# Optimization experiments

Hardware: AMD Instinct MI355X
Metric: run time of the kernel (lower is better)

Reference implementation:

```python
import jax, jax.numpy as jnp
import numpy as np

DECAY = 0.99
EPS = 1e-05


def setup_inputs() -> dict:
    key = jax.random.key(0)
    k1, k2, k3 = jax.random.split(key, 3)
    B, H, W, D, K = 16, 32, 32, 256, 8192
    x = jax.random.normal(k1, (B, H, W, D), dtype=jnp.float32)
    embed = jax.random.normal(k2, (D, K), dtype=jnp.float32)
    cluster_size = jnp.zeros((K,), dtype=jnp.float32)
    embed_avg = jax.random.normal(k3, (D, K), dtype=jnp.float32)
    return {"x": x, "embed": embed, "cluster_size": cluster_size, "embed_avg": embed_avg}


def reference(x, embed, cluster_size, embed_avg):
    D, K = embed.shape
    flat = x.reshape(-1, D)  # (N, D)
    # squared L2 distances: ||f||^2 - 2 f.e + ||e||^2  -> (N, K)
    dist = (flat * flat).sum(1, keepdims=True) - 2.0 * (flat @ embed) + (embed * embed).sum(0, keepdims=True)
    idx = jnp.argmin(dist, axis=1)  # (N,)
    quantize = jnp.take(embed.T, idx, axis=0).reshape(x.shape)  # (B,H,W,D)
    # EMA codebook statistics (training branch)
    onehot_sum = jnp.zeros((K,), dtype=flat.dtype).at[idx].add(1.0)  # (K,)
    embed_sum = jax.ops.segment_sum(flat, idx, num_segments=K).T  # (D, K)
    new_cluster_size = cluster_size * DECAY + (1.0 - DECAY) * onehot_sum
    new_embed_avg = embed_avg * DECAY + (1.0 - DECAY) * embed_sum
    n = new_cluster_size.sum()
    cs = (new_cluster_size + EPS) / (n + K * EPS) * n
    new_embed = new_embed_avg / cs[None, :]
    latent_loss = jnp.mean((jax.lax.stop_gradient(quantize) - x) ** 2)
    quantize_st = x + jax.lax.stop_gradient(quantize - x)  # straight-through
    return quantize_st, latent_loss, new_embed, new_cluster_size, new_embed_avg
```

## Files before the change

kernel.cpp:

```cpp
#include <hip/hip_runtime.h>

constexpr int NROWS = 16384;
constexpr int D     = 256;
constexpr int K     = 8192;

constexpr float DECAY = 0.99f;
constexpr float OMD   = 0.01f;
constexpr float EPSF  = 1e-5f;

constexpr size_t OUT_Q    = 0;
constexpr size_t OUT_LOSS = (size_t)NROWS * D;
constexpr size_t OUT_NE   = OUT_LOSS + 1;
constexpr size_t OUT_NCS  = OUT_NE + (size_t)D * K;
constexpr size_t OUT_NEA  = OUT_NCS + K;

constexpr size_t WS_KEYS  = 0;
constexpr size_t WS_ENORM = WS_KEYS + (size_t)NROWS * 8;
constexpr size_t WS_NSUM  = WS_ENORM + (size_t)K * 4;
constexpr size_t WS_XH    = ((WS_NSUM + 4096) / 4096) * 4096;
constexpr size_t WS_XL    = WS_XH + (size_t)NROWS * D * 2;
constexpr size_t WS_EHT   = WS_XL + (size_t)NROWS * D * 2;
constexpr size_t WS_ELT   = WS_EHT + (size_t)K * D * 2;

typedef unsigned int u32;
typedef unsigned short u16;
typedef unsigned long long u64;
typedef __attribute__((ext_vector_type(8))) short bf16x8;
typedef __attribute__((ext_vector_type(4))) float f32x4;
typedef __attribute__((ext_vector_type(4))) u32 u32x4;
typedef __attribute__((ext_vector_type(2))) u32 u32x2;

__device__ __forceinline__ u16 f2bf(float f) {
    u32 u = __float_as_uint(f);
    u32 r = (u + 0x7FFFu + ((u >> 16) & 1u)) >> 16;
    return (u16)r;
}
__device__ __forceinline__ float bf2f(u16 h) {
    return __uint_as_float((u32)h << 16);
}

__device__ __forceinline__ void gl_lds16(const void* g, void* l) {
    __builtin_amdgcn_global_load_lds(
        (const __attribute__((address_space(1))) u32*)g,
        (__attribute__((address_space(3))) u32*)l, 16, 0, 0);
}

__global__ void split_x_kernel(const float* __restrict__ x,
                               u16* __restrict__ xh, u16* __restrict__ xl) {
    size_t g = (size_t)blockIdx.x * blockDim.x + threadIdx.x;
    float4 v = *(const float4*)&x[g * 4];
    u16 h0 = f2bf(v.x), h1 = f2bf(v.y), h2 = f2bf(v.z), h3 = f2bf(v.w);
    u16 l0 = f2bf(v.x - bf2f(h0)), l1 = f2bf(v.y - bf2f(h1));
    u16 l2 = f2bf(v.z - bf2f(h2)), l3 = f2bf(v.w - bf2f(h3));
    u32x2 hp, lp;
    hp.x = (u32)h0 | ((u32)h1 << 16); hp.y = (u32)h2 | ((u32)h3 << 16);
    lp.x = (u32)l0 | ((u32)l1 << 16); lp.y = (u32)l2 | ((u32)l3 << 16);
    ((u32x2*)xh)[g] = hp;
    ((u32x2*)xl)[g] = lp;
}

__global__ void transpose_split_enorm(const float* __restrict__ embed,
                                      u16* __restrict__ ehT, u16* __restrict__ elT,
                                      float* __restrict__ enorm) {
    __shared__ float tile[64][68];
    const int kBase = blockIdx.x * 64;
    const int t  = threadIdx.x;
    const int dl = t >> 2;
    const int kl = t >> 2;
    const int qq = t & 3;
    float nacc = 0.f;

    for (int dBase = 0; dBase < D; dBase += 64) {
        #pragma unroll
        for (int i = 0; i < 4; ++i) {
            int kk = qq * 16 + i * 4;
            float4 v = *(const float4*)&embed[(size_t)(dBase + dl) * K + kBase + kk];
            tile[dl][kk + 0] = v.x; tile[dl][kk + 1] = v.y;
            tile[dl][kk + 2] = v.z; tile[dl][kk + 3] = v.w;
        }
        __syncthreads();
        u32 hp[8], lp[8];
        float s = 0.f;
        #pragma unroll
        for (int j = 0; j < 16; ++j) {
            float f = tile[qq * 16 + j][kl];
            s = fmaf(f, f, s);
            u16 hb = f2bf(f);
            u16 lb = f2bf(f - bf2f(hb));
            if (j & 1) { hp[j >> 1] |= (u32)hb << 16; lp[j >> 1] |= (u32)lb << 16; }
            else       { hp[j >> 1]  = hb;            lp[j >> 1]  = lb; }
        }
        s += __shfl_down(s, 1);
        s += __shfl_down(s, 2);
        if (qq == 0) nacc += s;

        size_t o = ((size_t)(kBase + kl) * D + dBase + qq * 16) >> 1;
        u32x4 a, b;
        a.x = hp[0]; a.y = hp[1]; a.z = hp[2]; a.w = hp[3];
        b.x = hp[4]; b.y = hp[5]; b.z = hp[6]; b.w = hp[7];
        *(u32x4*)&((u32*)ehT)[o]     = a;
        *(u32x4*)&((u32*)ehT)[o + 4] = b;
        a.x = lp[0]; a.y = lp[1]; a.z = lp[2]; a.w = lp[3];
        b.x = lp[4]; b.y = lp[5]; b.z = lp[6]; b.w = lp[7];
        *(u32x4*)&((u32*)elT)[o]     = a;
        *(u32x4*)&((u32*)elT)[o + 4] = b;
        __syncthreads();
    }
    if (qq == 0) enorm[kBase + kl] = nacc;
}

__global__ void cs_init_sum_kernel(const float* __restrict__ cluster_size,
                                   float* __restrict__ ncs_out,
                                   float* __restrict__ nsum) {
    int i = blockIdx.x * blockDim.x + threadIdx.x;
    float v = cluster_size[i];
    ncs_out[i] = DECAY * v;
    #pragma unroll
    for (int off = 32; off > 0; off >>= 1) v += __shfl_down(v, off);
    __shared__ float wsum[4];
    if ((threadIdx.x & 63) == 0) wsum[threadIdx.x >> 6] = v;
    __syncthreads();
    if (threadIdx.x == 0)
        atomicAdd(nsum, wsum[0] + wsum[1] + wsum[2] + wsum[3]);
}

__global__ __launch_bounds__(512, 2) void dist_argmin_mfma(
        const u16* __restrict__ xh, const u16* __restrict__ xl,
        const u16* __restrict__ ehT, const u16* __restrict__ elT,
        const float* __restrict__ enorm,
        u64* __restrict__ keys) {
    __shared__ u16 lds[2][32768];

    const int tid  = threadIdx.x;
    const int lane = tid & 63;
    const int wave = tid >> 6;
    const int wm   = wave >> 1;
    const int wn   = wave & 1;
    const int r = lane & 15, g = lane >> 4;
    const int rowBase = blockIdx.y * 256;
    const int colBase = blockIdx.x * 256;

    f32x4 acc[4][8];
    #pragma unroll
    for (int i = 0; i < 4; ++i)
        #pragma unroll
        for (int j = 0; j < 8; ++j) acc[i][j] = (f32x4)0.f;

    const int chunk8 = (((tid & 3) ^ ((tid >> 3) & 3)) * 8);
    const int arow   = tid >> 2;
    const size_t a0 = (size_t)(rowBase + arow) * D + chunk8;
    const size_t a1 = (size_t)(rowBase + 128 + arow) * D + chunk8;
    const int bmat   = tid >> 8;
    const int qrow   = (tid & 255) >> 2;
    const int bcol0  = (qrow < 32) ? qrow : (96 + qrow);
    const size_t bq0 = (size_t)(colBase + bcol0) * D + chunk8;
    const u16* bsrc  = bmat ? elT : ehT;

    const int kx = (g ^ ((r >> 1) & 3)) * 8;

    #define ST_XH0(buf, ks) gl_lds16(&xh[a0 + (ks) * 32], &lds[buf][tid * 8])
    #define ST_XH1(buf, ks) gl_lds16(&xh[a1 + (ks) * 32], &lds[buf][4096 + tid * 8])
    #define ST_XL0(buf, ks) gl_lds16(&xl[a0 + (ks) * 32], &lds[buf][8192 + tid * 8])
    #define ST_XL1(buf, ks) gl_lds16(&xl[a1 + (ks) * 32], &lds[buf][12288 + tid * 8])
    #define ST_B(buf, ks, q) \
        gl_lds16(&bsrc[bq0 + (size_t)(q) * 32 * D + (ks) * 32], \
                 &lds[buf][16384 + (q) * 4096 + tid * 8])

    ST_B(0, 0, 0); ST_XH0(0, 0); ST_B(0, 0, 1); ST_XH1(0, 0);
    ST_B(0, 0, 2); ST_XL0(0, 0); ST_B(0, 0, 3); ST_XL1(0, 0);
    ST_B(1, 1, 0); ST_XH0(1, 1); ST_B(1, 1, 1); ST_XH1(1, 1);
    ST_B(1, 1, 2); ST_XL0(1, 1);

    bf16x8 fah[4], fal[4], fbh[2], fbl[2];

    #define MFMA3(i, j, jj)                                                          \
        acc[i][j] = __builtin_amdgcn_mfma_f32_16x16x32_bf16(fah[i], fbh[jj], acc[i][j], 0, 0, 0); \
        acc[i][j] = __builtin_amdgcn_mfma_f32_16x16x32_bf16(fah[i], fbl[jj], acc[i][j], 0, 0, 0); \
        acc[i][j] = __builtin_amdgcn_mfma_f32_16x16x32_bf16(fal[i], fbh[jj], acc[i][j], 0, 0, 0)

    #pragma unroll
    for (int ks = 0; ks < 8; ++ks) {
        const int c = ks & 1;
        const u16* L = lds[c];

        if (ks == 7) asm volatile("s_waitcnt vmcnt(0)" ::: "memory");
        else         asm volatile("s_waitcnt vmcnt(6)" ::: "memory");
        __builtin_amdgcn_s_barrier();
        __builtin_amdgcn_sched_barrier(0);

        #pragma unroll
        for (int i = 0; i < 4; ++i) {
            fah[i] = *(const bf16x8*)&L[((wm * 64 + i * 16 + r) * 32) + kx];
            fal[i] = *(const bf16x8*)&L[8192 + ((wm * 64 + i * 16 + r) * 32) + kx];
        }
        #pragma unroll
        for (int jj = 0; jj < 2; ++jj) {
            const int qr = wn * 32 + jj * 16 + r;
            fbh[jj] = *(const bf16x8*)&L[16384 + qr * 32 + kx];
            fbl[jj] = *(const bf16x8*)&L[16384 + 2048 + qr * 32 + kx];
        }
        if (ks <= 6) { ST_B(c ^ 1, ks + 1, 3); ST_XL1(c ^ 1, ks + 1); }
        asm volatile("s_waitcnt lgkmcnt(0)" ::: "memory");
        __builtin_amdgcn_sched_barrier(0);
        __builtin_amdgcn_s_setprio(1);
        #pragma unroll
        for (int i = 0; i < 4; ++i) { MFMA3(i, 0, 0); MFMA3(i, 1, 1); }
        __builtin_amdgcn_s_setprio(0);
        __builtin_amdgcn_s_barrier();
        __builtin_amdgcn_sched_barrier(0);

        #pragma unroll
        for (int p = 1; p < 4; ++p) {
            #pragma unroll
            for (int jj = 0; jj < 2; ++jj) {
                const int qr = wn * 32 + jj * 16 + r;
                fbh[jj] = *(const bf16x8*)&L[16384 + p * 4096 + qr * 32 + kx];
                fbl[jj] = *(const bf16x8*)&L[16384 + p * 4096 + 2048 + qr * 32 + kx];
            }
            if (ks <= 5) {
                ST_B(c, ks + 2, p - 1);
                if      (p == 1) ST_XH0(c, ks + 2);
                else if (p == 2) ST_XH1(c, ks + 2);
                else             ST_XL0(c, ks + 2);
            }
            asm volatile("s_waitcnt lgkmcnt(0)" ::: "memory");
            __builtin_amdgcn_sched_barrier(0);
            __builtin_amdgcn_s_setprio(1);
            #pragma unroll
            for (int i = 0; i < 4; ++i) { MFMA3(i, 2 * p, 0); MFMA3(i, 2 * p + 1, 1); }
            __builtin_amdgcn_s_setprio(0);
            __builtin_amdgcn_s_barrier();
            __builtin_amdgcn_sched_barrier(0);
        }
    }
    #undef MFMA3
    #undef ST_XH0
    #undef ST_XH1
    #undef ST_XL0
    #undef ST_XL1
    #undef ST_B

    float en[8];
    #pragma unroll
    for (int j = 0; j < 8; ++j) en[j] = enorm[colBase + wn * 128 + j * 16 + r];

    #pragma unroll
    for (int i = 0; i < 4; ++i) {
        #pragma unroll
        for (int p4 = 0; p4 < 4; ++p4) {
            float best = __builtin_inff();
            int bk = 0;
            #pragma unroll
            for (int j = 0; j < 8; ++j) {
                float s = fmaf(-2.f, acc[i][j][p4], en[j]);
                int ccol = colBase + wn * 128 + j * 16 + r;
                if (s < best) { best = s; bk = ccol; }
            }
            u32 u = __float_as_uint(best);
            u ^= (u >> 31) ? 0xFFFFFFFFu : 0x80000000u;
            u64 key = ((u64)u << 32) | (u32)bk;
            #pragma unroll
            for (int m = 1; m < 16; m <<= 1) {
                u64 o = __shfl_xor(key, m);
                key = o < key ? o : key;
            }
            if (r == 0)
                atomicMin(&keys[rowBase + wm * 64 + i * 16 + g * 4 + p4], key);
        }
    }
}

__global__ void postprocess_kernel(const float* __restrict__ x,
                                   const u16* __restrict__ ehT,
                                   const u16* __restrict__ elT,
                                   const u64* __restrict__ keys,
                                   float* __restrict__ q_out,
                                   float* __restrict__ loss_out,
                                   float* __restrict__ acc_t,
                                   float* __restrict__ ncs_out) {
    const int w    = threadIdx.x >> 6;
    const int lane = threadIdx.x & 63;
    const int r    = blockIdx.x * 4 + w;
    const u32 k = (u32)keys[r];

    float4 xv = *(const float4*)&x[(size_t)r * D + lane * 4];
    size_t uo = ((size_t)k * D >> 1) + lane * 2;
    u32x2 hp = *(const u32x2*)&((const u32*)ehT)[uo];
    u32x2 lp = *(const u32x2*)&((const u32*)elT)[uo];
    float q0 = __uint_as_float(hp.x << 16)         + __uint_as_float(lp.x << 16);
    float q1 = __uint_as_float(hp.x & 0xFFFF0000u) + __uint_as_float(lp.x & 0xFFFF0000u);
    float q2 = __uint_as_float(hp.y << 16)         + __uint_as_float(lp.y << 16);
    float q3 = __uint_as_float(hp.y & 0xFFFF0000u) + __uint_as_float(lp.y & 0xFFFF0000u);
    *(float4*)&q_out[(size_t)r * D + lane * 4] = make_float4(q0, q1, q2, q3);

    float* dst = &acc_t[(size_t)k * D + lane * 4];
    atomicAdd(dst + 0, xv.x);
    atomicAdd(dst + 1, xv.y);
    atomicAdd(dst + 2, xv.z);
    atomicAdd(dst + 3, xv.w);
    if (lane == 0) atomicAdd(&ncs_out[k], OMD);

    float d0 = q0 - xv.x, d1 = q1 - xv.y, d2 = q2 - xv.z, d3 = q3 - xv.w;
    float lsum = fmaf(d0, d0, fmaf(d1, d1, fmaf(d2, d2, d3 * d3)));
    #pragma unroll
    for (int off = 32; off > 0; off >>= 1) lsum += __shfl_down(lsum, off);
    __shared__ float wsum[4];
    if (lane == 0) wsum[w] = lsum;
    __syncthreads();
    if (threadIdx.x == 0) {
        float s = wsum[0] + wsum[1] + wsum[2] + wsum[3];
        atomicAdd(loss_out, s * (1.0f / ((float)NROWS * (float)D)));
    }
}

__global__ void ema_finalize_kernel(const float* __restrict__ embed_avg,
                                    const float* __restrict__ acc_t,
                                    const float* __restrict__ ncs_out,
                                    const float* __restrict__ nsum,
                                    float* __restrict__ nea_out,
                                    float* __restrict__ ne_out) {
    __shared__ float tile[64][68];
    const int kBase = blockIdx.x * 64;
    const int dBase = blockIdx.y * 64;
    const int t = threadIdx.x;
    {
        const int kl = t >> 2, q = t & 3;
        #pragma unroll
        for (int i = 0; i < 4; ++i) {
            int dd = q * 16 + i * 4;
            float4 v = *(const float4*)&acc_t[(size_t)(kBase + kl) * D + dBase + dd];
            tile[kl][dd + 0] = v.x; tile[kl][dd + 1] = v.y;
            tile[kl][dd + 2] = v.z; tile[kl][dd + 3] = v.w;
        }
    }
    __syncthreads();
    const int dl = t >> 2, q = t & 3;
    const float n = DECAY * (*nsum) + OMD * (float)NROWS;
    const float inv_na = 1.0f / (n + (float)K * EPSF);
    #pragma unroll
    for (int i = 0; i < 4; ++i) {
        int kk = q * 16 + i * 4;
        size_t o = (size_t)(dBase + dl) * K + kBase + kk;
        float4 ea = *(const float4*)&embed_avg[o];
        float4 nea, ne;
        #pragma unroll
        for (int c = 0; c < 4; ++c) {
            float v  = DECAY * ((const float*)&ea)[c] + OMD * tile[kk + c][dl];
            float cs = (ncs_out[kBase + kk + c] + EPSF) * inv_na * n;
            ((float*)&nea)[c] = v;
            ((float*)&ne)[c]  = v / cs;
        }
        *(float4*)&nea_out[o] = nea;
        *(float4*)&ne_out[o]  = ne;
    }
}

extern "C" void kernel_launch(void* const* d_in, const int* in_sizes, int n_in,
                              void* d_out, int out_size, void* d_ws, size_t ws_size,
                              hipStream_t stream) {
    (void)in_sizes; (void)n_in; (void)out_size; (void)ws_size;
    const float* x            = (const float*)d_in[0];
    const float* embed        = (const float*)d_in[1];
    const float* cluster_size = (const float*)d_in[2];
    const float* embed_avg    = (const float*)d_in[3];
    float* out = (float*)d_out;

    char* ws = (char*)d_ws;
    u64*   keys  = (u64*)(ws + WS_KEYS);
    float* enorm = (float*)(ws + WS_ENORM);
    float* nsum  = (float*)(ws + WS_NSUM);
    u16*   xh    = (u16*)(ws + WS_XH);
    u16*   xl    = (u16*)(ws + WS_XL);
    u16*   ehT   = (u16*)(ws + WS_EHT);
    u16*   elT   = (u16*)(ws + WS_ELT);
    float* acc_t = (float*)(ws + WS_XH);

    float* q_out    = out + OUT_Q;
    float* loss_out = out + OUT_LOSS;
    float* ne_out   = out + OUT_NE;
    float* ncs_out  = out + OUT_NCS;
    float* nea_out  = out + OUT_NEA;

    hipMemsetAsync(keys, 0xFF, (size_t)NROWS * 8, stream);
    hipMemsetAsync(nsum, 0, 4, stream);
    hipMemsetAsync(loss_out, 0, 4, stream);

    split_x_kernel<<<dim3(NROWS * D / 4 / 256), dim3(256), 0, stream>>>(x, xh, xl);
    transpose_split_enorm<<<dim3(K / 64), dim3(256), 0, stream>>>(
        embed, ehT, elT, enorm);
    cs_init_sum_kernel<<<dim3(K / 256), dim3(256), 0, stream>>>(
        cluster_size, ncs_out, nsum);

    dist_argmin_mfma<<<dim3(K / 256, NROWS / 256), dim3(512), 0, stream>>>(
        xh, xl, ehT, elT, enorm, keys);

    hipMemsetAsync(acc_t, 0, (size_t)K * D * 4, stream);
    postprocess_kernel<<<dim3(NROWS / 4), dim3(256), 0, stream>>>(
        x, ehT, elT, keys, q_out, loss_out, acc_t, ncs_out);
    ema_finalize_kernel<<<dim3(K / 64, D / 64), dim3(256), 0, stream>>>(
        embed_avg, acc_t, ncs_out, nsum, nea_out, ne_out);
}
```

Measured before the change: 344.3 us.

## Simplify GEMM prefetch to one-stage double buffering with fewer barriers

Replaces the interleaved two-stage-ahead prefetch, which issued global-to-LDS loads between sub-steps and synchronised after each of four sub-steps, with a simpler scheme. Each k-step now issues all eight loads for the next buffer up front, waits, and runs all four MFMA sub-steps with only one barrier at the end. The intent is to cut barrier and waitcnt overhead inside the hot loop. In exchange the prefetch distance shrinks from two k-steps to one, so global latency may be less well hidden. The explicit lgkmcnt waits are also removed, leaving LDS read ordering to the compiler.

```diff
diff --git a/kernel.cpp b/kernel.cpp
--- a/kernel.cpp
+++ b/kernel.cpp
@@ -165,11 +165,15 @@
     #define ST_B(buf, ks, q) \
         gl_lds16(&bsrc[bq0 + (size_t)(q) * 32 * D + (ks) * 32], \
                  &lds[buf][16384 + (q) * 4096 + tid * 8])
-
-    ST_B(0, 0, 0); ST_XH0(0, 0); ST_B(0, 0, 1); ST_XH1(0, 0);
-    ST_B(0, 0, 2); ST_XL0(0, 0); ST_B(0, 0, 3); ST_XL1(0, 0);
-    ST_B(1, 1, 0); ST_XH0(1, 1); ST_B(1, 1, 1); ST_XH1(1, 1);
-    ST_B(1, 1, 2); ST_XL0(1, 1);
+    #define ST_ALL(buf, ks)                                        \
+        do {                                                       \
+            ST_B(buf, ks, 0); ST_XH0(buf, ks);                     \
+            ST_B(buf, ks, 1); ST_XH1(buf, ks);                     \
+            ST_B(buf, ks, 2); ST_XL0(buf, ks);                     \
+            ST_B(buf, ks, 3); ST_XL1(buf, ks);                     \
+        } while (0)
+
+    ST_ALL(0, 0);
 
     bf16x8 fah[4], fal[4], fbh[2], fbl[2];
 
@@ -183,8 +187,12 @@
         const int c = ks & 1;
         const u16* L = lds[c];
 
-        if (ks == 7) asm volatile("s_waitcnt vmcnt(0)" ::: "memory");
-        else         asm volatile("s_waitcnt vmcnt(6)" ::: "memory");
+        if (ks < 7) {
+            ST_ALL(c ^ 1, ks + 1);
+            asm volatile("s_waitcnt vmcnt(8)" ::: "memory");
+        } else {
+            asm volatile("s_waitcnt vmcnt(0)" ::: "memory");
+        }
         __builtin_amdgcn_s_barrier();
         __builtin_amdgcn_sched_barrier(0);
 
@@ -194,46 +202,23 @@
             fal[i] = *(const bf16x8*)&L[8192 + ((wm * 64 + i * 16 + r) * 32) + kx];
         }
         #pragma unroll
-        for (int jj = 0; jj < 2; ++jj) {
-            const int qr = wn * 32 + jj * 16 + r;
-            fbh[jj] = *(const bf16x8*)&L[16384 + qr * 32 + kx];
-            fbl[jj] = *(const bf16x8*)&L[16384 + 2048 + qr * 32 + kx];
-        }
-        if (ks <= 6) { ST_B(c ^ 1, ks + 1, 3); ST_XL1(c ^ 1, ks + 1); }
-        asm volatile("s_waitcnt lgkmcnt(0)" ::: "memory");
-        __builtin_amdgcn_sched_barrier(0);
-        __builtin_amdgcn_s_setprio(1);
-        #pragma unroll
-        for (int i = 0; i < 4; ++i) { MFMA3(i, 0, 0); MFMA3(i, 1, 1); }
-        __builtin_amdgcn_s_setprio(0);
-        __builtin_amdgcn_s_barrier();
-        __builtin_amdgcn_sched_barrier(0);
-
-        #pragma unroll
-        for (int p = 1; p < 4; ++p) {
+        for (int p = 0; p < 4; ++p) {
             #pragma unroll
             for (int jj = 0; jj < 2; ++jj) {
                 const int qr = wn * 32 + jj * 16 + r;
                 fbh[jj] = *(const bf16x8*)&L[16384 + p * 4096 + qr * 32 + kx];
                 fbl[jj] = *(const bf16x8*)&L[16384 + p * 4096 + 2048 + qr * 32 + kx];
             }
-            if (ks <= 5) {
-                ST_B(c, ks + 2, p - 1);
-                if      (p == 1) ST_XH0(c, ks + 2);
-                else if (p == 2) ST_XH1(c, ks + 2);
-                else             ST_XL0(c, ks + 2);
-            }
-            asm volatile("s_waitcnt lgkmcnt(0)" ::: "memory");
-            __builtin_amdgcn_sched_barrier(0);
             __builtin_amdgcn_s_setprio(1);
             #pragma unroll
             for (int i = 0; i < 4; ++i) { MFMA3(i, 2 * p, 0); MFMA3(i, 2 * p + 1, 1); }
             __builtin_amdgcn_s_setprio(0);
-            __builtin_amdgcn_s_barrier();
-            __builtin_amdgcn_sched_barrier(0);
-        }
+        }
+        __builtin_amdgcn_sched_barrier(0);
+        __builtin_amdgcn_s_barrier();
     }
     #undef MFMA3
+    #undef ST_ALL
     #undef ST_XH0
     #undef ST_XH1
     #undef ST_XL0
```

Result: slower. 361.7 us (+5.1%).
